# Kernel tuning notes

Hardware: AMD Instinct MI355X
Metric: run time of the kernel (lower is better)

Reference implementation:

```python
import jax, jax.numpy as jnp
import numpy as np

EPS = 1e-5
K = 32

def _bn(x, g, b, m, v):
    # eval-mode BatchNorm over channel (last) axis
    return (x - m) * jax.lax.rsqrt(v + EPS) * g + b

def _attn_pool(x, sw, sb, mw, mb):
    # x: [B, N, C]; scores softmax over N
    s = jax.nn.softmax(jnp.einsum('bnc,oc->bno', x, sw) + sb, axis=1)  # [B,N,1]
    pooled = jnp.sum(s * x, axis=1)  # [B,C]
    return pooled @ mw.T + mb

def setup_inputs() -> dict:
    key = jax.random.key(0)
    ks = jax.random.split(key, 16)
    B, N, G = 8, 8192, 512
    d = {}
    d['xyz'] = jax.random.normal(ks[0], (B, N, 3), jnp.float32)
    d['center_idx'] = jax.random.randint(ks[1], (B, G), 0, N, jnp.int64)
    s = lambda k, shp, f: (jax.random.normal(k, shp, jnp.float32) * f)
    d['w1'] = s(ks[2], (128, 10), 0.3); d['b1'] = jnp.zeros((128,))
    d['g1'] = jnp.ones((128,)); d['be1'] = jnp.zeros((128,))
    d['m1'] = jnp.zeros((128,)); d['v1'] = jnp.ones((128,))
    d['w2'] = s(ks[3], (256, 128), 0.08); d['b2'] = jnp.zeros((256,))
    d['ap1_sw'] = s(ks[4], (1, 256), 0.06); d['ap1_sb'] = jnp.zeros((1,))
    d['ap1_mw'] = s(ks[5], (256, 256), 0.06); d['ap1_mb'] = jnp.zeros((256,))
    d['w3'] = s(ks[6], (512, 512), 0.04); d['b3'] = jnp.zeros((512,))
    d['g2'] = jnp.ones((512,)); d['be2'] = jnp.zeros((512,))
    d['m2'] = jnp.zeros((512,)); d['v2'] = jnp.ones((512,))
    d['w4'] = s(ks[7], (512, 512), 0.04); d['b4'] = jnp.zeros((512,))
    d['ap2_sw'] = s(ks[8], (1, 512), 0.04); d['ap2_sb'] = jnp.zeros((1,))
    d['ap2_mw'] = s(ks[9], (512, 512), 0.04); d['ap2_mb'] = jnp.zeros((512,))
    return d

def reference(xyz, center_idx, w1, b1, g1, be1, m1, v1, w2, b2,
              ap1_sw, ap1_sb, ap1_mw, ap1_mb, w3, b3, g2, be2, m2, v2,
              w4, b4, ap2_sw, ap2_sb, ap2_mw, ap2_mb):
    B, N, _ = xyz.shape
    G = center_idx.shape[1]
    # center sampling (replaces misc.random_sample with explicit indices)
    center = jnp.take_along_axis(xyz, center_idx[..., None], axis=1)  # [B,G,3]
    # knn: squared pairwise distances, top-k smallest
    d2 = (jnp.sum(center**2, -1)[:, :, None] + jnp.sum(xyz**2, -1)[:, None, :]
          - 2.0 * jnp.einsum('bgc,bnc->bgn', center, xyz))  # [B,G,N]
    _, idx = jax.lax.top_k(-d2, K)  # [B,G,K]
    neighborhood = jax.vmap(lambda pts, i: pts[i])(xyz, idx)  # [B,G,K,3]
    xyz_tile = jnp.broadcast_to(center[:, :, None, :], (B, G, K, 3))
    rel = xyz_tile - neighborhood
    rdist = jnp.sqrt(jnp.sum(rel**2, -1, keepdims=True))
    feat = jnp.concatenate([rdist, rel, xyz_tile, neighborhood], -1)  # [B,G,K,10]
    x = feat.reshape(B * G, K, 10)
    # first_conv: 1x1 convs == per-point linear
    x = jax.nn.relu(_bn(jnp.einsum('bnc,oc->bno', x, w1) + b1, g1, be1, m1, v1))
    x = jnp.einsum('bnc,oc->bno', x, w2) + b2  # [BG,K,256]
    fg = _attn_pool(x, ap1_sw, ap1_sb, ap1_mw, ap1_mb)  # [BG,256]
    x = jnp.concatenate([jnp.broadcast_to(fg[:, None, :], x.shape), x], -1)  # [BG,K,512]
    x = jax.nn.relu(_bn(jnp.einsum('bnc,oc->bno', x, w3) + b3, g2, be2, m2, v2))
    x = jnp.einsum('bnc,oc->bno', x, w4) + b4  # [BG,K,512]
    fg2 = _attn_pool(x, ap2_sw, ap2_sb, ap2_mw, ap2_mb)  # [BG,512]
    return center, fg2.reshape(B, G, 512)
```

## Files before the change

kernel.cpp:

```cpp
#include <hip/hip_runtime.h>
#include <math.h>

#define EPSV 1e-5f

typedef __attribute__((ext_vector_type(8))) short bf16x8;
typedef __attribute__((ext_vector_type(4))) float f32x4;

#define MFMA16(a, b, c) __builtin_amdgcn_mfma_f32_16x16x32_bf16(a, b, c, 0, 0, 0)

__device__ __forceinline__ short f2bf(float x) {
    unsigned u = __float_as_uint(x);
    unsigned r = (u + 0x7fffu + ((u >> 16) & 1u)) >> 16;
    return (short)r;
}
__device__ __forceinline__ float bf2f(short h) {
    return __uint_as_float(((unsigned)(unsigned short)h) << 16);
}
__device__ __forceinline__ void bsplit(float x, short& h, short& l) {
    h = f2bf(x);
    l = f2bf(x - bf2f(h));
}

#define KCAP 2048
__global__ __launch_bounds__(256) void prep_knn(
    const float* __restrict__ xyz, const int* __restrict__ cidx,
    int* __restrict__ knn_idx, float* __restrict__ out_center,
    const float* __restrict__ w1, const float* __restrict__ b1,
    const float* __restrict__ w2, const float* __restrict__ w3,
    const float* __restrict__ mw1, const float* __restrict__ mw2,
    const float* __restrict__ w4, const float* __restrict__ b4,
    const float* __restrict__ sw2, const float* __restrict__ sb2,
    const float* __restrict__ mb2, const float* __restrict__ mb1,
    const float* __restrict__ b3,
    const float* __restrict__ g1, const float* __restrict__ be1,
    const float* __restrict__ m1, const float* __restrict__ v1,
    const float* __restrict__ g2, const float* __restrict__ be2,
    const float* __restrict__ m2, const float* __restrict__ v2,
    short* __restrict__ w1fh, short* __restrict__ w2fh, short* __restrict__ w3fh,
    short* __restrict__ Pfh, short* __restrict__ MTfh,
    float* __restrict__ sc1, float* __restrict__ shb1,
    float* __restrict__ sc2, float* __restrict__ sh2,
    float* __restrict__ u, float* __restrict__ bb, float* __restrict__ ub,
    float* __restrict__ bc3)
{
    __shared__ __align__(16) char shm[12416];
    int B = blockIdx.x, t = threadIdx.x;
    int lane = t & 63, w = t >> 6;

    if (B < 4096) {
        unsigned* cu = (unsigned*)shm;
        unsigned short* cix = (unsigned short*)(shm + 8192);
        unsigned* Tws = (unsigned*)(shm + 12288);
        unsigned* cntS = (unsigned*)(shm + 12304);
        int g = B, b = g >> 9;
        const float* xb = xyz + (size_t)b * 8192 * 3;
        int ci = cidx[g];
        float cx = xb[ci * 3 + 0], cy = xb[ci * 3 + 1], cz = xb[ci * 3 + 2];
        float c2 = cx * cx + cy * cy + cz * cz;
        if (t < 3) out_center[g * 3 + t] = xb[ci * 3 + t];
        if (t == 0) *cntS = 0;

        const float4* p4 = (const float4*)xb + (size_t)t * 24;
        unsigned ue[32];
        unsigned vmin = 0xffffffffu;
        #pragma unroll
        for (int ii = 0; ii < 8; ++ii) {
            float4 v0 = p4[ii * 3 + 0];
            float4 v1 = p4[ii * 3 + 1];
            float4 v2 = p4[ii * 3 + 2];
            float px[4], py[4], pz[4];
            px[0] = v0.x; py[0] = v0.y; pz[0] = v0.z;
            px[1] = v0.w; py[1] = v1.x; pz[1] = v1.y;
            px[2] = v1.z; py[2] = v1.w; pz[2] = v2.x;
            px[3] = v2.y; py[3] = v2.z; pz[3] = v2.w;
            #pragma unroll
            for (int m = 0; m < 4; ++m) {
                float dx = px[m], dy = py[m], dz = pz[m];
                float n2 = dx * dx + dy * dy + dz * dz;
                float d = c2 + n2 - 2.f * (cx * dx + cy * dy + cz * dz);
                unsigned uu = __float_as_uint(d);
                uu = (uu & 0x80000000u) ? ~uu : (uu | 0x80000000u);
                ue[ii * 4 + m] = uu;
                vmin = min(vmin, uu);
            }
        }
        unsigned v = vmin;
        #pragma unroll
        for (int k = 2; k <= 64; k <<= 1) {
            #pragma unroll
            for (int jj = k >> 1; jj > 0; jj >>= 1) {
                unsigned o = __shfl_xor(v, jj);
                bool dir_asc = ((lane & k) == 0) || (k == 64);
                bool lower = (lane & jj) == 0;
                bool take_min = (lower == dir_asc);
                unsigned mn = min(v, o), mx = max(v, o);
                v = take_min ? mn : mx;
            }
        }
        unsigned Tw = __shfl(v, 31);
        if (lane == 0) Tws[w] = Tw;
        __syncthreads();
        unsigned T = min(min(Tws[0], Tws[1]), min(Tws[2], Tws[3]));
        #pragma unroll
        for (int i = 0; i < 32; ++i) {
            if (ue[i] <= T) {
                unsigned pos = atomicAdd(cntS, 1u);
                if (pos < KCAP) {
                    cu[pos] = ue[i];
                    cix[pos] = (unsigned short)(t * 32 + i);
                }
            }
        }
        __syncthreads();
        int C = (int)min(*cntS, (unsigned)KCAP);
        for (int cc = t; cc < C; cc += 256) {
            unsigned uc = cu[cc];
            unsigned short icd = cix[cc];
            int rank = 0;
            for (int j = 0; j < C; ++j) {
                unsigned uj = cu[j];
                rank += (uj < uc) || (uj == uc && cix[j] < icd);
            }
            if (rank < 32) knn_idx[g * 32 + rank] = (int)icd;
        }
        return;
    }

    if (B < 4352) {
        float* col = (float*)shm;
        int c = B - 4096;
        col[t] = mw1[t * 256 + c];
        __syncthreads();
        int ks = c >> 5, qq = (c >> 3) & 3, jj = c & 7;
        for (int oo = t; oo < 512; oo += 256) {
            float acc = 0.f;
            for (int d = 0; d < 256; ++d) acc += col[d] * w3[oo * 512 + d];
            int ct = oo >> 4;
            size_t idx = ((size_t)(ct * 8 + ks) * 64 + qq * 16 + (oo & 15)) * 8 + jj;
            Pfh[idx] = f2bf(acc);
        }
        return;
    }

    if (B < 4864) {
        float* row = (float*)shm;
        int qq = B - 4352;
        row[t] = mw2[(size_t)qq * 512 + t];
        row[t + 256] = mw2[(size_t)qq * 512 + t + 256];
        __syncthreads();
        float a0 = 0.f, a1 = 0.f;
        for (int o = 0; o < 512; ++o) {
            float m = row[o];
            a0 += m * w4[o * 512 + t];
            a1 += m * w4[o * 512 + t + 256];
        }
        int ct = qq >> 4, nl = qq & 15;
        {
            int k = t;
            size_t i0 = (((size_t)(ct * 16 + (k >> 5))) << 9)
                      | ((((k >> 3) & 3) * 16 + nl) << 3) | (k & 7);
            MTfh[i0] = f2bf(a0);
        }
        {
            int k = t + 256;
            size_t i1 = (((size_t)(ct * 16 + (k >> 5))) << 9)
                      | ((((k >> 3) & 3) * 16 + nl) << 3) | (k & 7);
            MTfh[i1] = f2bf(a1);
        }
        return;
    }

    if (B < 4992) {
        int tid = (B - 4864) * 256 + t;
        {
            int i = tid;
            int j = i & 7, ln = (i >> 3) & 63, rest = i >> 9;
            int ks = rest & 3, ct = rest >> 2;
            int o = ct * 16 + (ln & 15);
            int k = ks * 32 + (ln >> 4) * 8 + j;
            w2fh[i] = f2bf(w2[o * 128 + k]);
        }
        #pragma unroll
        for (int s = 0; s < 4; ++s) {
            int i = tid + s * 32768;
            int j = i & 7, ln = (i >> 3) & 63, rest = i >> 9;
            int ks = rest & 7, ct = rest >> 3;
            int o = ct * 16 + (ln & 15);
            int c = 256 + ks * 32 + (ln >> 4) * 8 + j;
            w3fh[i] = f2bf(w3[o * 512 + c]);
        }
        return;
    }

    if (B < 5056) {
        float* b4s = (float*)shm;
        float* red = (float*)(shm + 2048);
        b4s[t] = b4[t];
        b4s[t + 256] = b4[t + 256];
        __syncthreads();
        int q0 = (B - 4992) * 8;
        for (int i = 0; i < 8; ++i) {
            int q = q0 + i;
            float part = mw2[(size_t)q * 512 + t] * b4s[t]
                       + mw2[(size_t)q * 512 + 256 + t] * b4s[256 + t];
            #pragma unroll
            for (int off = 32; off > 0; off >>= 1) part += __shfl_down(part, off);
            if (lane == 0) red[w] = part;
            __syncthreads();
            if (t == 0) bb[q] = mb2[q] + red[0] + red[1] + red[2] + red[3];
            __syncthreads();
        }
        return;
    }

    if (B < 5120) {
        float* mb1s = (float*)shm;
        float* red = (float*)(shm + 1024);
        mb1s[t] = mb1[t];
        __syncthreads();
        int o0 = (B - 5056) * 8;
        for (int i = 0; i < 8; ++i) {
            int o = o0 + i;
            float part = w3[(size_t)o * 512 + t] * mb1s[t];
            #pragma unroll
            for (int off = 32; off > 0; off >>= 1) part += __shfl_down(part, off);
            if (lane == 0) red[w] = part;
            __syncthreads();
            if (t == 0) bc3[o] = b3[o] + red[0] + red[1] + red[2] + red[3];
            __syncthreads();
        }
        return;
    }

    if (B < 5122) {
        int c = (B - 5120) * 256 + t;
        float acc = 0.f;
        for (int o = 0; o < 512; ++o) acc += sw2[o] * w4[o * 512 + c];
        u[c] = acc;
        return;
    }

    if (t < 128) {
        float s = g1[t] * rsqrtf(v1[t] + EPSV);
        float sh = be1[t] - m1[t] * s;
        sc1[t] = s;
        shb1[t] = b1[t] * s + sh;
    }
    {
        float s = g2[t] * rsqrtf(v2[t] + EPSV);
        sc2[t] = s; sh2[t] = be2[t] - m2[t] * s;
        s = g2[t + 256] * rsqrtf(v2[t + 256] + EPSV);
        sc2[t + 256] = s; sh2[t + 256] = be2[t + 256] - m2[t + 256] * s;
    }
    #pragma unroll
    for (int s = 0; s < 16; ++s) {
        int i = t + s * 256;
        int j = i & 7, ln = (i >> 3) & 63, ct = i >> 9;
        int o = ct * 16 + (ln & 15);
        int k = (ln >> 4) * 8 + j;
        w1fh[i] = (k < 10) ? f2bf(w1[o * 10 + k]) : (short)0;
    }
    if (t < 64) {
        float part = 0.f;
        #pragma unroll
        for (int i = 0; i < 8; ++i) part += sw2[t * 8 + i] * b4[t * 8 + i];
        #pragma unroll
        for (int off = 32; off > 0; off >>= 1) part += __shfl_down(part, off);
        if (t == 0) ub[0] = sb2[0] + part;
    }
}

__global__ __launch_bounds__(512) void mlp_kernel(
    const float* __restrict__ xyz, const int* __restrict__ cidx,
    const int* __restrict__ knn_idx,
    const short* __restrict__ w1fh,
    const float* __restrict__ sc1, const float* __restrict__ shb1,
    const short* __restrict__ w2fh,
    const float* __restrict__ b2,
    const float* __restrict__ sw1, const float* __restrict__ sb1,
    const short* __restrict__ Pfh, const float* __restrict__ bc3,
    const short* __restrict__ w3fh,
    const float* __restrict__ sc2, const float* __restrict__ sh2,
    const float* __restrict__ u, const float* __restrict__ ubp,
    short* __restrict__ yh)
{
    __shared__ __align__(16) char smem[70784];
    short* x1 = (short*)smem;
    short* x2 = (short*)smem;
    short* feat_h = (short*)(smem + 32768);
    short* feat_l = (short*)(smem + 40960);
    short* poolA  = (short*)(smem + 65536);
    float* cen  = (float*)(smem + 69632);
    float* scs  = (float*)(smem + 69696);
    float* sms  = (float*)(smem + 70208);

    int gb = blockIdx.x * 4;
    int bq = gb >> 9;
    int t = threadIdx.x;
    int lane = t & 63, wv = t >> 6, q = lane >> 4, r = lane & 15;
    const float* xb = xyz + (size_t)bq * 8192 * 3;

    if (t < 4) {
        int ci = cidx[gb + t];
        cen[t * 3 + 0] = xb[ci * 3 + 0];
        cen[t * 3 + 1] = xb[ci * 3 + 1];
        cen[t * 3 + 2] = xb[ci * 3 + 2];
    }
    if (t < 128) scs[t] = sb1[0];
    __syncthreads();

    if (t < 128) {
        int gg = t >> 5, kk = t & 31;
        int n = knn_idx[(gb + gg) * 32 + kk];
        float cxx = cen[gg * 3 + 0], cyy = cen[gg * 3 + 1], czz = cen[gg * 3 + 2];
        float nx = xb[n * 3 + 0], ny = xb[n * 3 + 1], nz = xb[n * 3 + 2];
        float rx = cxx - nx, ry = cyy - ny, rz = czz - nz;
        float rd = sqrtf(rx * rx + ry * ry + rz * rz);
        float f[10];
        f[0] = rd; f[1] = rx; f[2] = ry; f[3] = rz;
        f[4] = cxx; f[5] = cyy; f[6] = czz;
        f[7] = nx; f[8] = ny; f[9] = nz;
        short* fh = feat_h + t * 32;
        short* fl = feat_l + t * 32;
        #pragma unroll
        for (int c = 0; c < 10; ++c) {
            short h, l; bsplit(f[c], h, l);
            fh[c] = h; fl[c] = l;
        }
        #pragma unroll
        for (int c = 10; c < 32; ++c) { fh[c] = 0; fl[c] = 0; }
    }
    __syncthreads();

    {
        f32x4 acc1[8];
        #pragma unroll
        for (int rt = 0; rt < 8; ++rt) acc1[rt] = (f32x4){0.f, 0.f, 0.f, 0.f};
        bf16x8 bw = *(const bf16x8*)(w1fh + ((size_t)wv * 64 + lane) * 8);
        #pragma unroll
        for (int rt = 0; rt < 8; ++rt) {
            int row = rt * 16 + r;
            bf16x8 ah = *(const bf16x8*)(feat_h + row * 32 + q * 8);
            bf16x8 al = *(const bf16x8*)(feat_l + row * 32 + q * 8);
            acc1[rt] = MFMA16(al, bw, acc1[rt]);
            acc1[rt] = MFMA16(ah, bw, acc1[rt]);
        }
        int o = wv * 16 + r;
        float s1v = sc1[o], sbv = shb1[o];
        #pragma unroll
        for (int rt = 0; rt < 8; ++rt)
            #pragma unroll
            for (int j = 0; j < 4; ++j) {
                int row = rt * 16 + q * 4 + j;
                float vv = fmaxf(acc1[rt][j] * s1v + sbv, 0.f);
                x1[row * 128 + (o ^ ((row & 7) << 3))] = f2bf(vv);
            }
    }
    __syncthreads();

    f32x4 acc2[8][2];
    #pragma unroll
    for (int rt = 0; rt < 8; ++rt)
        #pragma unroll
        for (int ctl = 0; ctl < 2; ++ctl) {
            float bv = b2[(wv * 2 + ctl) * 16 + r];
            acc2[rt][ctl] = (f32x4){bv, bv, bv, bv};
        }
    #pragma unroll
    for (int ks = 0; ks < 4; ++ks) {
        bf16x8 af[8];
        #pragma unroll
        for (int rt = 0; rt < 8; ++rt) {
            int row = rt * 16 + r;
            int kk = ks * 32 + q * 8;
            af[rt] = *(const bf16x8*)(x1 + row * 128 + (kk ^ ((row & 7) << 3)));
        }
        #pragma unroll
        for (int ctl = 0; ctl < 2; ++ctl) {
            int ct = wv * 2 + ctl;
            size_t woff = ((size_t)(ct * 4 + ks) * 64 + lane) * 8;
            bf16x8 bh = *(const bf16x8*)(w2fh + woff);
            #pragma unroll
            for (int rt = 0; rt < 8; ++rt)
                acc2[rt][ctl] = MFMA16(af[rt], bh, acc2[rt][ctl]);
        }
    }
    {
        float sw1v[2];
        #pragma unroll
        for (int ctl = 0; ctl < 2; ++ctl) sw1v[ctl] = sw1[(wv * 2 + ctl) * 16 + r];
        #pragma unroll
        for (int rt = 0; rt < 8; ++rt)
            #pragma unroll
            for (int j = 0; j < 4; ++j) {
                float s = sw1v[0] * acc2[rt][0][j] + sw1v[1] * acc2[rt][1][j];
                s += __shfl_xor(s, 1); s += __shfl_xor(s, 2);
                s += __shfl_xor(s, 4); s += __shfl_xor(s, 8);
                if (r == 0) atomicAdd(&scs[rt * 16 + q * 4 + j], s);
            }
    }
    __syncthreads();

    if (wv < 4 && lane < 32) {
        float s = scs[wv * 32 + lane];
        float mx = s;
        mx = fmaxf(mx, __shfl_xor(mx, 16));
        mx = fmaxf(mx, __shfl_xor(mx, 8));
        mx = fmaxf(mx, __shfl_xor(mx, 4));
        mx = fmaxf(mx, __shfl_xor(mx, 2));
        mx = fmaxf(mx, __shfl_xor(mx, 1));
        float e = expf(s - mx);
        float sum = e;
        sum += __shfl_xor(sum, 16);
        sum += __shfl_xor(sum, 8);
        sum += __shfl_xor(sum, 4);
        sum += __shfl_xor(sum, 2);
        sum += __shfl_xor(sum, 1);
        sms[wv * 32 + lane] = e / sum;
    }
    #pragma unroll
    for (int rt = 0; rt < 8; ++rt)
        #pragma unroll
        for (int ctl = 0; ctl < 2; ++ctl) {
            int ch = (wv * 2 + ctl) * 16 + r;
            #pragma unroll
            for (int j = 0; j < 4; ++j) {
                int row = rt * 16 + q * 4 + j;
                x2[row * 256 + (ch ^ ((row & 7) << 3))] = f2bf(acc2[rt][ctl][j]);
            }
        }
    __syncthreads();

    {
        #pragma unroll
        for (int ctl = 0; ctl < 2; ++ctl)
            #pragma unroll
            for (int gg = 0; gg < 4; ++gg) {
                float p = 0.f;
                #pragma unroll
                for (int rr = 0; rr < 2; ++rr) {
                    int rt = gg * 2 + rr;
                    #pragma unroll
                    for (int j = 0; j < 4; ++j)
                        p += sms[rt * 16 + q * 4 + j] * acc2[rt][ctl][j];
                }
                p += __shfl_xor(p, 16);
                p += __shfl_xor(p, 32);
                if (q == 0) {
                    int ch = (wv * 2 + ctl) * 16 + r;
                    short h, l; bsplit(p, h, l);
                    poolA[gg * 256 + (ch ^ (gg << 3))] = h;
                    poolA[(gg + 4) * 256 + (ch ^ ((gg + 4) << 3))] = l;
                }
            }
        if (t < 128) scs[t] = ubp[0];
    }
    __syncthreads();

    float fgv[4][4];
    float bc3v[4];
    {
        f32x4 accP[4];
        #pragma unroll
        for (int ctl = 0; ctl < 4; ++ctl) accP[ctl] = (f32x4){0.f, 0.f, 0.f, 0.f};
        #pragma unroll
        for (int ks = 0; ks < 8; ++ks) {
            int kk = ks * 32 + q * 8;
            bf16x8 pa;
            if (r < 8) pa = *(const bf16x8*)(poolA + r * 256 + (kk ^ (r << 3)));
            else pa = (bf16x8){0, 0, 0, 0, 0, 0, 0, 0};
            #pragma unroll
            for (int ctl = 0; ctl < 4; ++ctl) {
                size_t woff = ((size_t)((wv * 4 + ctl) * 8 + ks) * 64 + lane) * 8;
                bf16x8 ph = *(const bf16x8*)(Pfh + woff);
                accP[ctl] = MFMA16(pa, ph, accP[ctl]);
            }
        }
        #pragma unroll
        for (int ctl = 0; ctl < 4; ++ctl) {
            bc3v[ctl] = bc3[(wv * 4 + ctl) * 16 + r];
            #pragma unroll
            for (int j = 0; j < 4; ++j) {
                float x = accP[ctl][j];
                x += __shfl_xor(x, 16);
                x += __shfl_xor(x, 32);
                fgv[ctl][j] = x;
            }
        }
    }

    f32x4 acc3[8][4];
    #pragma unroll
    for (int rt = 0; rt < 8; ++rt) {
        int gg = rt >> 1;
        #pragma unroll
        for (int ctl = 0; ctl < 4; ++ctl) {
            float fp = fgv[ctl][gg] + bc3v[ctl];
            acc3[rt][ctl] = (f32x4){fp, fp, fp, fp};
        }
    }
    #pragma unroll
    for (int ks = 0; ks < 8; ++ks) {
        bf16x8 af[8];
        #pragma unroll
        for (int rt = 0; rt < 8; ++rt) {
            int row = rt * 16 + r;
            int kk = ks * 32 + q * 8;
            af[rt] = *(const bf16x8*)(x2 + row * 256 + (kk ^ ((row & 7) << 3)));
        }
        #pragma unroll
        for (int ctl = 0; ctl < 4; ++ctl) {
            int ct = wv * 4 + ctl;
            size_t woff = ((size_t)(ct * 8 + ks) * 64 + lane) * 8;
            bf16x8 bh = *(const bf16x8*)(w3fh + woff);
            #pragma unroll
            for (int rt = 0; rt < 8; ++rt)
                acc3[rt][ctl] = MFMA16(af[rt], bh, acc3[rt][ctl]);
        }
    }
    float uv[4];
    {
        #pragma unroll
        for (int ctl = 0; ctl < 4; ++ctl) {
            int ch = (wv * 4 + ctl) * 16 + r;
            float s = sc2[ch], sh = sh2[ch];
            uv[ctl] = u[ch];
            #pragma unroll
            for (int rt = 0; rt < 8; ++rt)
                #pragma unroll
                for (int j = 0; j < 4; ++j)
                    acc3[rt][ctl][j] = fmaxf(acc3[rt][ctl][j] * s + sh, 0.f);
        }
        #pragma unroll
        for (int rt = 0; rt < 8; ++rt)
            #pragma unroll
            for (int j = 0; j < 4; ++j) {
                float s = uv[0] * acc3[rt][0][j] + uv[1] * acc3[rt][1][j]
                        + uv[2] * acc3[rt][2][j] + uv[3] * acc3[rt][3][j];
                s += __shfl_xor(s, 1); s += __shfl_xor(s, 2);
                s += __shfl_xor(s, 4); s += __shfl_xor(s, 8);
                if (r == 0) atomicAdd(&scs[rt * 16 + q * 4 + j], s);
            }
    }
    __syncthreads();

    if (wv < 4 && lane < 32) {
        float s = scs[wv * 32 + lane];
        float mx = s;
        mx = fmaxf(mx, __shfl_xor(mx, 16));
        mx = fmaxf(mx, __shfl_xor(mx, 8));
        mx = fmaxf(mx, __shfl_xor(mx, 4));
        mx = fmaxf(mx, __shfl_xor(mx, 2));
        mx = fmaxf(mx, __shfl_xor(mx, 1));
        float e = expf(s - mx);
        float sum = e;
        sum += __shfl_xor(sum, 16);
        sum += __shfl_xor(sum, 8);
        sum += __shfl_xor(sum, 4);
        sum += __shfl_xor(sum, 2);
        sum += __shfl_xor(sum, 1);
        sms[wv * 32 + lane] = e / sum;
    }
    __syncthreads();

    {
        #pragma unroll
        for (int ctl = 0; ctl < 4; ++ctl)
            #pragma unroll
            for (int gg = 0; gg < 4; ++gg) {
                float p = 0.f;
                #pragma unroll
                for (int rr = 0; rr < 2; ++rr) {
                    int rt = gg * 2 + rr;
                    #pragma unroll
                    for (int j = 0; j < 4; ++j)
                        p += sms[rt * 16 + q * 4 + j] * acc3[rt][ctl][j];
                }
                p += __shfl_xor(p, 16);
                p += __shfl_xor(p, 32);
                if (q == 0) {
                    int grow = gb + gg;
                    int ch = (wv * 4 + ctl) * 16 + r;
                    yh[(size_t)grow * 512 + ch] = f2bf(p);
                }
            }
    }
}

__global__ __launch_bounds__(256) void fg2_kernel(
    const short* __restrict__ yh,
    const short* __restrict__ MTfh,
    const float* __restrict__ bb, float* __restrict__ out_fg2)
{
    int gbase = blockIdx.x * 16;
    int t = threadIdx.x;
    int lane = t & 63, wv = t >> 6, q = lane >> 4, r = lane & 15;
    f32x4 acc[8];
    #pragma unroll
    for (int ctl = 0; ctl < 8; ++ctl) {
        float bv = bb[(wv * 8 + ctl) * 16 + r];
        acc[ctl] = (f32x4){bv, bv, bv, bv};
    }
    #pragma unroll
    for (int ks = 0; ks < 16; ++ks) {
        bf16x8 af = *(const bf16x8*)(yh + (size_t)(gbase + r) * 512 + ks * 32 + q * 8);
        #pragma unroll
        for (int ctl = 0; ctl < 8; ++ctl) {
            int ct = wv * 8 + ctl;
            size_t woff = ((size_t)(ct * 16 + ks) * 64 + lane) * 8;
            bf16x8 bh = *(const bf16x8*)(MTfh + woff);
            acc[ctl] = MFMA16(af, bh, acc[ctl]);
        }
    }
    #pragma unroll
    for (int ctl = 0; ctl < 8; ++ctl) {
        int ch = (wv * 8 + ctl) * 16 + r;
        #pragma unroll
        for (int j = 0; j < 4; ++j) {
            int grow = gbase + q * 4 + j;
            out_fg2[(size_t)grow * 512 + ch] = acc[ctl][j];
        }
    }
}

extern "C" void kernel_launch(void* const* d_in, const int* in_sizes, int n_in,
                              void* d_out, int out_size, void* d_ws, size_t ws_size,
                              hipStream_t stream) {
    const float* xyz  = (const float*)d_in[0];
    const int*   cidx = (const int*)d_in[1];
    const float* w1   = (const float*)d_in[2];
    const float* b1   = (const float*)d_in[3];
    const float* g1   = (const float*)d_in[4];
    const float* be1  = (const float*)d_in[5];
    const float* m1   = (const float*)d_in[6];
    const float* v1   = (const float*)d_in[7];
    const float* w2   = (const float*)d_in[8];
    const float* b2   = (const float*)d_in[9];
    const float* sw1  = (const float*)d_in[10];
    const float* sb1  = (const float*)d_in[11];
    const float* mw1  = (const float*)d_in[12];
    const float* mb1  = (const float*)d_in[13];
    const float* w3   = (const float*)d_in[14];
    const float* b3   = (const float*)d_in[15];
    const float* g2   = (const float*)d_in[16];
    const float* be2  = (const float*)d_in[17];
    const float* m2   = (const float*)d_in[18];
    const float* v2   = (const float*)d_in[19];
    const float* w4   = (const float*)d_in[20];
    const float* b4   = (const float*)d_in[21];
    const float* sw2  = (const float*)d_in[22];
    const float* sb2  = (const float*)d_in[23];
    const float* mw2  = (const float*)d_in[24];
    const float* mb2  = (const float*)d_in[25];

    float* out = (float*)d_out;
    char* ws = (char*)d_ws;
    int*   knn_idx = (int*)(ws + 0);
    short* w2fh = (short*)(ws + 524288);
    short* w3fh = (short*)(ws + 655360);
    short* Pfh  = (short*)(ws + 1179648);
    short* w1fh = (short*)(ws + 1441792);
    float* bc3  = (float*)(ws + 1703936);
    float* sc1  = (float*)(ws + 1705984);
    float* shb1 = (float*)(ws + 1706496);
    float* sc2  = (float*)(ws + 1707008);
    float* sh2  = (float*)(ws + 1709056);
    float* u    = (float*)(ws + 1711104);
    float* bb   = (float*)(ws + 1713152);
    float* ub   = (float*)(ws + 1715200);
    short* MTfh = (short*)(ws + 1715456);
    short* yh   = (short*)(ws + 2764032);

    prep_knn<<<5123, 256, 0, stream>>>(xyz, cidx, knn_idx, out,
                                       w1, b1, w2, w3, mw1, mw2, w4, b4, sw2, sb2,
                                       mb2, mb1, b3,
                                       g1, be1, m1, v1, g2, be2, m2, v2,
                                       w1fh, w2fh, w3fh, Pfh, MTfh,
                                       sc1, shb1, sc2, sh2, u, bb, ub, bc3);
    mlp_kernel<<<1024, 512, 0, stream>>>(xyz, cidx, knn_idx,
                                         w1fh, sc1, shb1, w2fh, b2,
                                         sw1, sb1, Pfh, bc3, w3fh,
                                         sc2, sh2, u, ub, yh);
    fg2_kernel<<<256, 256, 0, stream>>>(yh, MTfh, bb, out + 12288);
}
```

Baseline: 336.6 us.

## Fuse KNN selection into MLP kernel and shrink feature LDS buffers

Moves the per-center KNN search out of the prep kernel and into the MLP kernel, where each 512-thread block handles its 4 centers in sequence. This removes the knn_idx global round trip and the 4096 KNN blocks from the prep launch. Feature hi/lo bf16 parts are packed into one padded buffer, and zero-padded K-slices are skipped by predicating the loads. The cost is a serial four-pass KNN inside each MLP block with extra barriers, which lengthens that kernel, and a launch-bounds occupancy hint that may constrain registers.

Result: slower. 872.8 us (+159.3%).

```diff
diff --git a/kernel.cpp b/kernel.cpp
--- a/kernel.cpp
+++ b/kernel.cpp
@@ -20,11 +20,11 @@
     h = f2bf(x);
     l = f2bf(x - bf2f(h));
 }
-
-#define KCAP 2048
-__global__ __launch_bounds__(256) void prep_knn(
-    const float* __restrict__ xyz, const int* __restrict__ cidx,
-    int* __restrict__ knn_idx, float* __restrict__ out_center,
+__device__ __forceinline__ unsigned pack2(short a, short b) {
+    return ((unsigned)(unsigned short)a) | (((unsigned)(unsigned short)b) << 16);
+}
+
+__global__ __launch_bounds__(256) void prep_kernel(
     const float* __restrict__ w1, const float* __restrict__ b1,
     const float* __restrict__ w2, const float* __restrict__ w3,
     const float* __restrict__ mw1, const float* __restrict__ mw2,
@@ -43,92 +43,13 @@
     float* __restrict__ u, float* __restrict__ bb, float* __restrict__ ub,
     float* __restrict__ bc3)
 {
-    __shared__ __align__(16) char shm[12416];
+    __shared__ __align__(16) float shm[520];
     int B = blockIdx.x, t = threadIdx.x;
     int lane = t & 63, w = t >> 6;
 
-    if (B < 4096) {
-        unsigned* cu = (unsigned*)shm;
-        unsigned short* cix = (unsigned short*)(shm + 8192);
-        unsigned* Tws = (unsigned*)(shm + 12288);
-        unsigned* cntS = (unsigned*)(shm + 12304);
-        int g = B, b = g >> 9;
-        const float* xb = xyz + (size_t)b * 8192 * 3;
-        int ci = cidx[g];
-        float cx = xb[ci * 3 + 0], cy = xb[ci * 3 + 1], cz = xb[ci * 3 + 2];
-        float c2 = cx * cx + cy * cy + cz * cz;
-        if (t < 3) out_center[g * 3 + t] = xb[ci * 3 + t];
-        if (t == 0) *cntS = 0;
-
-        const float4* p4 = (const float4*)xb + (size_t)t * 24;
-        unsigned ue[32];
-        unsigned vmin = 0xffffffffu;
-        #pragma unroll
-        for (int ii = 0; ii < 8; ++ii) {
-            float4 v0 = p4[ii * 3 + 0];
-            float4 v1 = p4[ii * 3 + 1];
-            float4 v2 = p4[ii * 3 + 2];
-            float px[4], py[4], pz[4];
-            px[0] = v0.x; py[0] = v0.y; pz[0] = v0.z;
-            px[1] = v0.w; py[1] = v1.x; pz[1] = v1.y;
-            px[2] = v1.z; py[2] = v1.w; pz[2] = v2.x;
-            px[3] = v2.y; py[3] = v2.z; pz[3] = v2.w;
-            #pragma unroll
-            for (int m = 0; m < 4; ++m) {
-                float dx = px[m], dy = py[m], dz = pz[m];
-                float n2 = dx * dx + dy * dy + dz * dz;
-                float d = c2 + n2 - 2.f * (cx * dx + cy * dy + cz * dz);
-                unsigned uu = __float_as_uint(d);
-                uu = (uu & 0x80000000u) ? ~uu : (uu | 0x80000000u);
-                ue[ii * 4 + m] = uu;
-                vmin = min(vmin, uu);
-            }
-        }
-        unsigned v = vmin;
-        #pragma unroll
-        for (int k = 2; k <= 64; k <<= 1) {
-            #pragma unroll
-            for (int jj = k >> 1; jj > 0; jj >>= 1) {
-                unsigned o = __shfl_xor(v, jj);
-                bool dir_asc = ((lane & k) == 0) || (k == 64);
-                bool lower = (lane & jj) == 0;
-                bool take_min = (lower == dir_asc);
-                unsigned mn = min(v, o), mx = max(v, o);
-                v = take_min ? mn : mx;
-            }
-        }
-        unsigned Tw = __shfl(v, 31);
-        if (lane == 0) Tws[w] = Tw;
-        __syncthreads();
-        unsigned T = min(min(Tws[0], Tws[1]), min(Tws[2], Tws[3]));
-        #pragma unroll
-        for (int i = 0; i < 32; ++i) {
-            if (ue[i] <= T) {
-                unsigned pos = atomicAdd(cntS, 1u);
-                if (pos < KCAP) {
-                    cu[pos] = ue[i];
-                    cix[pos] = (unsigned short)(t * 32 + i);
-                }
-            }
-        }
-        __syncthreads();
-        int C = (int)min(*cntS, (unsigned)KCAP);
-        for (int cc = t; cc < C; cc += 256) {
-            unsigned uc = cu[cc];
-            unsigned short icd = cix[cc];
-            int rank = 0;
-            for (int j = 0; j < C; ++j) {
-                unsigned uj = cu[j];
-                rank += (uj < uc) || (uj == uc && cix[j] < icd);
-            }
-            if (rank < 32) knn_idx[g * 32 + rank] = (int)icd;
-        }
-        return;
-    }
-
-    if (B < 4352) {
-        float* col = (float*)shm;
-        int c = B - 4096;
+    if (B < 256) {
+        float* col = shm;
+        int c = B;
         col[t] = mw1[t * 256 + c];
         __syncthreads();
         int ks = c >> 5, qq = (c >> 3) & 3, jj = c & 7;
@@ -142,9 +63,9 @@
         return;
     }
 
-    if (B < 4864) {
-        float* row = (float*)shm;
-        int qq = B - 4352;
+    if (B < 768) {
+        float* row = shm;
+        int qq = B - 256;
         row[t] = mw2[(size_t)qq * 512 + t];
         row[t + 256] = mw2[(size_t)qq * 512 + t + 256];
         __syncthreads();
@@ -170,8 +91,8 @@
         return;
     }
 
-    if (B < 4992) {
-        int tid = (B - 4864) * 256 + t;
+    if (B < 896) {
+        int tid = (B - 768) * 256 + t;
         {
             int i = tid;
             int j = i & 7, ln = (i >> 3) & 63, rest = i >> 9;
@@ -192,13 +113,13 @@
         return;
     }
 
-    if (B < 5056) {
-        float* b4s = (float*)shm;
-        float* red = (float*)(shm + 2048);
+    if (B < 960) {
+        float* b4s = shm;
+        float* red = shm + 512;
         b4s[t] = b4[t];
         b4s[t + 256] = b4[t + 256];
         __syncthreads();
-        int q0 = (B - 4992) * 8;
+        int q0 = (B - 896) * 8;
         for (int i = 0; i < 8; ++i) {
             int q = q0 + i;
             float part = mw2[(size_t)q * 512 + t] * b4s[t]
@@ -213,12 +134,12 @@
         return;
     }
 
-    if (B < 5120) {
-        float* mb1s = (float*)shm;
-        float* red = (float*)(shm + 1024);
+    if (B < 1024) {
+        float* mb1s = shm;
+        float* red = shm + 512;
         mb1s[t] = mb1[t];
         __syncthreads();
-        int o0 = (B - 5056) * 8;
+        int o0 = (B - 960) * 8;
         for (int i = 0; i < 8; ++i) {
             int o = o0 + i;
             float part = w3[(size_t)o * 512 + t] * mb1s[t];
@@ -232,8 +153,8 @@
         return;
     }
 
-    if (B < 5122) {
-        int c = (B - 5120) * 256 + t;
+    if (B < 1026) {
+        int c = (B - 1024) * 256 + t;
         float acc = 0.f;
         for (int o = 0; o < 512; ++o) acc += sw2[o] * w4[o * 512 + c];
         u[c] = acc;
@@ -270,9 +191,10 @@
     }
 }
 
-__global__ __launch_bounds__(512) void mlp_kernel(
+#define KCAP 2048
+__global__ __launch_bounds__(512, 4) void mlp_kernel(
     const float* __restrict__ xyz, const int* __restrict__ cidx,
-    const int* __restrict__ knn_idx,
+    float* __restrict__ out_center,
     const short* __restrict__ w1fh,
     const float* __restrict__ sc1, const float* __restrict__ shb1,
     const short* __restrict__ w2fh,
@@ -284,15 +206,18 @@
     const float* __restrict__ u, const float* __restrict__ ubp,
     short* __restrict__ yh)
 {
-    __shared__ __align__(16) char smem[70784];
+    __shared__ __align__(16) char smem[71296];
     short* x1 = (short*)smem;
     short* x2 = (short*)smem;
-    short* feat_h = (short*)(smem + 32768);
-    short* feat_l = (short*)(smem + 40960);
-    short* poolA  = (short*)(smem + 65536);
-    float* cen  = (float*)(smem + 69632);
-    float* scs  = (float*)(smem + 69696);
-    float* sms  = (float*)(smem + 70208);
+    unsigned* cu = (unsigned*)smem;
+    unsigned short* cix = (unsigned short*)(smem + 8192);
+    short* feat = (short*)(smem + 32768);
+    short* poolA = (short*)(smem + 65536);
+    float* scs = (float*)(smem + 69632);
+    float* sms = (float*)(smem + 70144);
+    int* kidx = (int*)(smem + 70656);
+    unsigned* Tws = (unsigned*)(smem + 71168);
+    unsigned* cntp = (unsigned*)(smem + 71200);
 
     int gb = blockIdx.x * 4;
     int bq = gb >> 9;
@@ -300,19 +225,88 @@
     int lane = t & 63, wv = t >> 6, q = lane >> 4, r = lane & 15;
     const float* xb = xyz + (size_t)bq * 8192 * 3;
 
-    if (t < 4) {
-        int ci = cidx[gb + t];
-        cen[t * 3 + 0] = xb[ci * 3 + 0];
-        cen[t * 3 + 1] = xb[ci * 3 + 1];
-        cen[t * 3 + 2] = xb[ci * 3 + 2];
-    }
-    if (t < 128) scs[t] = sb1[0];
-    __syncthreads();
+    if (t == 0) *cntp = 0;
+    for (int g = 0; g < 4; ++g) {
+        int gg = gb + g;
+        int ci = cidx[gg];
+        float cx = xb[ci * 3 + 0], cy = xb[ci * 3 + 1], cz = xb[ci * 3 + 2];
+        float c2 = cx * cx + cy * cy + cz * cz;
+        if (t < 3) out_center[gg * 3 + t] = xb[ci * 3 + t];
+
+        const float4* p4 = (const float4*)xb + (size_t)t * 12;
+        unsigned ue[16];
+        unsigned vmin = 0xffffffffu;
+        #pragma unroll
+        for (int ii = 0; ii < 4; ++ii) {
+            float4 v0 = p4[ii * 3 + 0];
+            float4 v1 = p4[ii * 3 + 1];
+            float4 v2 = p4[ii * 3 + 2];
+            float px[4], py[4], pz[4];
+            px[0] = v0.x; py[0] = v0.y; pz[0] = v0.z;
+            px[1] = v0.w; py[1] = v1.x; pz[1] = v1.y;
+            px[2] = v1.z; py[2] = v1.w; pz[2] = v2.x;
+            px[3] = v2.y; py[3] = v2.z; pz[3] = v2.w;
+            #pragma unroll
+            for (int m = 0; m < 4; ++m) {
+                float dx = px[m], dy = py[m], dz = pz[m];
+                float n2 = dx * dx + dy * dy + dz * dz;
+                float d = c2 + n2 - 2.f * (cx * dx + cy * dy + cz * dz);
+                unsigned uu = __float_as_uint(d);
+                uu = (uu & 0x80000000u) ? ~uu : (uu | 0x80000000u);
+                ue[ii * 4 + m] = uu;
+                vmin = min(vmin, uu);
+            }
+        }
+        unsigned v = vmin;
+        #pragma unroll
+        for (int k = 2; k <= 64; k <<= 1) {
+            #pragma unroll
+            for (int jj = k >> 1; jj > 0; jj >>= 1) {
+                unsigned o = __shfl_xor(v, jj);
+                bool dir_asc = ((lane & k) == 0) || (k == 64);
+                bool lower = (lane & jj) == 0;
+                bool take_min = (lower == dir_asc);
+                unsigned mn = min(v, o), mx = max(v, o);
+                v = take_min ? mn : mx;
+            }
+        }
+        unsigned Tw = __shfl(v, 31);
+        if (lane == 0) Tws[wv] = Tw;
+        __syncthreads();
+        unsigned T = Tws[0];
+        #pragma unroll
+        for (int j = 1; j < 8; ++j) T = min(T, Tws[j]);
+        #pragma unroll
+        for (int i = 0; i < 16; ++i) {
+            if (ue[i] <= T) {
+                unsigned pos = atomicAdd(cntp, 1u);
+                if (pos < KCAP) {
+                    cu[pos] = ue[i];
+                    cix[pos] = (unsigned short)(t * 16 + i);
+                }
+            }
+        }
+        __syncthreads();
+        int C = (int)min(*cntp, (unsigned)KCAP);
+        for (int cc = t; cc < C; cc += 512) {
+            unsigned uc = cu[cc];
+            unsigned short icd = cix[cc];
+            int rank = 0;
+            for (int j = 0; j < C; ++j) {
+                unsigned uj = cu[j];
+                rank += (uj < uc) || (uj == uc && cix[j] < icd);
+            }
+            if (rank < 32) kidx[g * 32 + rank] = (int)icd;
+        }
+        __syncthreads();
+        if (t == 0) *cntp = 0;
+    }
 
     if (t < 128) {
-        int gg = t >> 5, kk = t & 31;
-        int n = knn_idx[(gb + gg) * 32 + kk];
-        float cxx = cen[gg * 3 + 0], cyy = cen[gg * 3 + 1], czz = cen[gg * 3 + 2];
+        int gg = t >> 5;
+        int ci = cidx[gb + gg];
+        float cxx = xb[ci * 3 + 0], cyy = xb[ci * 3 + 1], czz = xb[ci * 3 + 2];
+        int n = kidx[t];
         float nx = xb[n * 3 + 0], ny = xb[n * 3 + 1], nz = xb[n * 3 + 2];
         float rx = cxx - nx, ry = cyy - ny, rz = czz - nz;
         float rd = sqrtf(rx * rx + ry * ry + rz * rz);
@@ -320,16 +314,19 @@
         f[0] = rd; f[1] = rx; f[2] = ry; f[3] = rz;
         f[4] = cxx; f[5] = cyy; f[6] = czz;
         f[7] = nx; f[8] = ny; f[9] = nz;
-        short* fh = feat_h + t * 32;
-        short* fl = feat_l + t * 32;
-        #pragma unroll
-        for (int c = 0; c < 10; ++c) {
-            short h, l; bsplit(f[c], h, l);
-            fh[c] = h; fl[c] = l;
-        }
-        #pragma unroll
-        for (int c = 10; c < 32; ++c) { fh[c] = 0; fl[c] = 0; }
-    }
+        unsigned* fr = (unsigned*)(feat + t * 40);
+        short h0, l0, h1, l1;
+        #pragma unroll
+        for (int c = 0; c < 10; c += 2) {
+            bsplit(f[c], h0, l0);
+            bsplit(f[c + 1], h1, l1);
+            fr[c >> 1] = pack2(h0, h1);
+            fr[8 + (c >> 1)] = pack2(l0, l1);
+        }
+        fr[5] = 0; fr[6] = 0; fr[7] = 0;
+        fr[13] = 0; fr[14] = 0; fr[15] = 0;
+    }
+    if (t < 128) scs[t] = sb1[0];
     __syncthreads();
 
     {
@@ -337,11 +334,15 @@
         #pragma unroll
         for (int rt = 0; rt < 8; ++rt) acc1[rt] = (f32x4){0.f, 0.f, 0.f, 0.f};
         bf16x8 bw = *(const bf16x8*)(w1fh + ((size_t)wv * 64 + lane) * 8);
+        bf16x8 zerov = (bf16x8){0, 0, 0, 0, 0, 0, 0, 0};
         #pragma unroll
         for (int rt = 0; rt < 8; ++rt) {
             int row = rt * 16 + r;
-            bf16x8 ah = *(const bf16x8*)(feat_h + row * 32 + q * 8);
-            bf16x8 al = *(const bf16x8*)(feat_l + row * 32 + q * 8);
+            bf16x8 ah = zerov, al = zerov;
+            if (q < 2) {
+                ah = *(const bf16x8*)(feat + row * 40 + q * 8);
+                al = *(const bf16x8*)(feat + row * 40 + 16 + q * 8);
+            }
             acc1[rt] = MFMA16(al, bw, acc1[rt]);
             acc1[rt] = MFMA16(ah, bw, acc1[rt]);
         }
@@ -655,7 +656,6 @@
 
     float* out = (float*)d_out;
     char* ws = (char*)d_ws;
-    int*   knn_idx = (int*)(ws + 0);
     short* w2fh = (short*)(ws + 524288);
     short* w3fh = (short*)(ws + 655360);
     short* Pfh  = (short*)(ws + 1179648);
@@ -671,13 +671,12 @@
     short* MTfh = (short*)(ws + 1715456);
     short* yh   = (short*)(ws + 2764032);
 
-    prep_knn<<<5123, 256, 0, stream>>>(xyz, cidx, knn_idx, out,
-                                       w1, b1, w2, w3, mw1, mw2, w4, b4, sw2, sb2,
-                                       mb2, mb1, b3,
-                                       g1, be1, m1, v1, g2, be2, m2, v2,
-                                       w1fh, w2fh, w3fh, Pfh, MTfh,
-                                       sc1, shb1, sc2, sh2, u, bb, ub, bc3);
-    mlp_kernel<<<1024, 512, 0, stream>>>(xyz, cidx, knn_idx,
+    prep_kernel<<<1027, 256, 0, stream>>>(w1, b1, w2, w3, mw1, mw2, w4, b4,
+                                          sw2, sb2, mb2, mb1, b3,
+                                          g1, be1, m1, v1, g2, be2, m2, v2,
+                                          w1fh, w2fh, w3fh, Pfh, MTfh,
+                                          sc1, shb1, sc2, sh2, u, bb, ub, bc3);
+    mlp_kernel<<<1024, 512, 0, stream>>>(xyz, cidx, out,
                                          w1fh, sc1, shb1, w2fh, b2,
                                          sw1, sb1, Pfh, bc3, w3fh,
                                          sc2, sh2, u, ub, yh);
```
